# Kernel tuning notes

Measured on AMD Instinct MI355X. Metric: run time of the kernel, lower is better.

The kernel has to match this reference:

```python
import jax, jax.numpy as jnp
import numpy as np

N_EMBD = 1024
N_HEAD = 16
HEAD_DIM = N_EMBD // N_HEAD


def setup_inputs() -> dict:
    key = jax.random.key(0)
    ks = jax.random.split(key, 5)
    B, S = 2, 2048
    scale = 0.02
    return {
        "hidden_states": jax.random.normal(ks[0], (B, S, N_EMBD), dtype=jnp.float32),
        "w_attn": jax.random.normal(ks[1], (N_EMBD, 3 * N_EMBD), dtype=jnp.float32) * scale,
        "b_attn": jnp.zeros((3 * N_EMBD,), dtype=jnp.float32),
        "w_proj": jax.random.normal(ks[2], (N_EMBD, N_EMBD), dtype=jnp.float32) * scale,
        "b_proj": jnp.zeros((N_EMBD,), dtype=jnp.float32),
    }


def reference(hidden_states, w_attn, b_attn, w_proj, b_proj):
    B, S, _ = hidden_states.shape
    qkv = hidden_states @ w_attn + b_attn                     # [B,S,3E]
    q, k, v = jnp.split(qkv, 3, axis=-1)                      # each [B,S,E]

    def split_heads(t):  # [B,S,E] -> [B,H,S,D]
        return t.reshape(B, S, N_HEAD, HEAD_DIM).transpose(0, 2, 1, 3)

    q, k, v = split_heads(q), split_heads(k), split_heads(v)

    scores = jnp.einsum("bhqd,bhkd->bhqk", q, k) / np.sqrt(HEAD_DIM).astype(np.float32)
    causal = jnp.tril(jnp.ones((S, S), dtype=bool))
    scores = jnp.where(causal[None, None], scores, jnp.float32(-jnp.inf))
    attn = jax.nn.softmax(scores, axis=-1)                    # [B,H,S,S]
    out = jnp.einsum("bhqk,bhkd->bhqd", attn, v)              # [B,H,S,D]
    out = out.transpose(0, 2, 1, 3).reshape(B, S, N_EMBD)     # merge heads
    out = out @ w_proj + b_proj
    return out
```

## Files before the change

kernel.cpp:

```cpp
#include <hip/hip_runtime.h>
#include <hip/hip_bf16.h>


typedef __attribute__((ext_vector_type(4))) float  float4v;
typedef __attribute__((ext_vector_type(8))) short  short8v;
typedef __attribute__((ext_vector_type(4))) short  short4v;

#define ATT_SCALE 0.18033688011112042f

__device__ __forceinline__ short f2bf(float f) {
  union { float f; unsigned u; } v; v.f = f;
  unsigned r = v.u + 0x7fffu + ((v.u >> 16) & 1u);
  return (short)(r >> 16);
}
__device__ __forceinline__ float bf2f(short s) {
  union { unsigned u; float f; } v; v.u = ((unsigned)(unsigned short)s) << 16;
  return v.f;
}

__device__ __forceinline__ short4v pack_bf16x4(float a, float b, float c, float d) {
  unsigned x0 = __builtin_bit_cast(unsigned, a) + 0x8000u;
  unsigned x1 = __builtin_bit_cast(unsigned, b) + 0x8000u;
  unsigned x2 = __builtin_bit_cast(unsigned, c) + 0x8000u;
  unsigned x3 = __builtin_bit_cast(unsigned, d) + 0x8000u;
  union { unsigned u[2]; short4v s; } r;
  r.u[0] = __builtin_amdgcn_perm(x1, x0, 0x07060302);
  r.u[1] = __builtin_amdgcn_perm(x3, x2, 0x07060302);
  return r.s;
}

__device__ __forceinline__ short4v cvt_pk_bf16x4(float a, float b, float c, float d) {
  union { unsigned u[2]; short4v s; } r;
  asm("v_cvt_pk_bf16_f32 %0, %1, %2" : "=v"(r.u[0]) : "v"(a), "v"(b));
  asm("v_cvt_pk_bf16_f32 %0, %1, %2" : "=v"(r.u[1]) : "v"(c), "v"(d));
  return r.s;
}

__device__ __forceinline__ void gl_lds16(const void* g, void* l) {
  __builtin_amdgcn_global_load_lds(
      (const __attribute__((address_space(1))) unsigned*)g,
      (__attribute__((address_space(3))) unsigned*)l, 16, 0, 0);
}

__global__ __launch_bounds__(256) void prep_kernel(
    const float* __restrict__ hidden, const float* __restrict__ w_attn,
    const float* __restrict__ w_proj, short* __restrict__ hA,
    short* __restrict__ wqkvT, short* __restrict__ wprojT) {
  __shared__ float tile[32][33];
  const int bx = blockIdx.x, t = threadIdx.x;
  if (bx < 4096) {
    const size_t i = ((size_t)bx * 256 + t) * 4;
    float4v v = *(const float4v*)(hidden + i);
    short4v o;
    #pragma unroll
    for (int k = 0; k < 4; k++) o[k] = f2bf(v[k]);
    *(short4v*)(hA + i) = o;
    return;
  }
  const float* in; short* out; int R, C, cx, cy;
  if (bx < 4096 + 3072) {
    in = w_attn; out = wqkvT; R = 1024; C = 3072;
    cx = (bx - 4096) % 96; cy = (bx - 4096) / 96;
  } else {
    in = w_proj; out = wprojT; R = 1024; C = 1024;
    cx = (bx - 7168) % 32; cy = (bx - 7168) / 32;
  }
  const int tx = t & 31, ty = t >> 5;
  const int c0 = cx * 32, r0 = cy * 32;
  #pragma unroll
  for (int i = 0; i < 4; i++)
    tile[ty + i * 8][tx] = in[(size_t)(r0 + ty + i * 8) * C + c0 + tx];
  __syncthreads();
  #pragma unroll
  for (int i = 0; i < 4; i++) {
    const int cc = ty + i * 8;
    out[(size_t)(c0 + cc) * R + r0 + tx] = f2bf(tile[tx][cc]);
  }
}

template<int RB, int MODE>
__global__ __launch_bounds__(256) void gemm_bt(
    const short* __restrict__ A, const short* __restrict__ Bt,
    const float* __restrict__ bias, void* __restrict__ Cout,
    short* __restrict__ vA, int M, int N, int K)
{
  __shared__ short As[3][RB][32];
  __shared__ short Bs[3][128][32];
  const int MI = RB / 32;
  const int t    = threadIdx.x;
  const int lane = t & 63;
  const int wave = t >> 6;
  const int wm   = (wave >> 1) * (RB / 2);
  const int wn   = (wave & 1) * 64;
  const int l16  = lane & 15;
  const int quad = lane >> 4;
  const int row0 = blockIdx.y * RB;
  const int col0 = blockIdx.x * 128;

  float4v acc[MI][4] = {};

  const int srow = lane >> 2;
  const int scol = (lane & 3) * 8;
  const int gcol = ((lane & 3) ^ ((srow >> 1) & 3)) * 8;
  const int rquad = (quad ^ ((l16 >> 1) & 3)) * 8;

  const short* gA0 = A + (size_t)(row0 + wave * ((RB == 128) ? 32 : 16) + srow) * K + gcol;
  const short* gA1 = gA0 + (size_t)16 * K;
  const short* gB0 = Bt + (size_t)(col0 + wave * 32 + srow) * K + gcol;
  const short* gB1 = gB0 + (size_t)16 * K;

  const int NI = K / 32;

  auto stage = [&](int kt, int b) {
    const int k0 = kt * 32;
    if (RB == 128) {
      gl_lds16(gA0 + k0, &As[b][wave * 32 + srow][scol]);
      gl_lds16(gA1 + k0, &As[b][wave * 32 + 16 + srow][scol]);
    } else {
      gl_lds16(gA0 + k0, &As[b][(wave * 16 + srow) & (RB - 1)][scol]);
    }
    gl_lds16(gB0 + k0, &Bs[b][wave * 32 + srow][scol]);
    gl_lds16(gB1 + k0, &Bs[b][wave * 32 + 16 + srow][scol]);
  };

  stage(0, 0);
  stage(1, 1);
  if (RB == 128) asm volatile("s_waitcnt vmcnt(4)" ::: "memory");
  else           asm volatile("s_waitcnt vmcnt(3)" ::: "memory");
  __builtin_amdgcn_s_barrier();
  __builtin_amdgcn_sched_barrier(0);

  int buf = 0;
  for (int i = 0; i < NI; i++) {
    if (i + 2 < NI) stage(i + 2, (buf + 2 >= 3) ? buf - 1 : buf + 2);

    short8v af[MI], bf[4];
    #pragma unroll
    for (int ii = 0; ii < MI; ii++)
      af[ii] = *(const short8v*)&As[buf][wm + ii * 16 + l16][rquad];
    #pragma unroll
    for (int j = 0; j < 4; j++)
      bf[j] = *(const short8v*)&Bs[buf][wn + j * 16 + l16][rquad];
    #pragma unroll
    for (int ii = 0; ii < MI; ii++)
      #pragma unroll
      for (int j = 0; j < 4; j++)
        acc[ii][j] = __builtin_amdgcn_mfma_f32_16x16x32_bf16(af[ii], bf[j], acc[ii][j], 0, 0, 0);

    if (i + 1 < NI) {
      if (i + 2 < NI) {
        if (RB == 128) asm volatile("s_waitcnt vmcnt(4)" ::: "memory");
        else           asm volatile("s_waitcnt vmcnt(3)" ::: "memory");
      } else {
        asm volatile("s_waitcnt vmcnt(0)" ::: "memory");
      }
      __builtin_amdgcn_s_barrier();
      __builtin_amdgcn_sched_barrier(0);
    }
    buf = (buf >= 2) ? 0 : buf + 1;
  }

  if (MODE == 2 && col0 >= 2048) {
    const int b  = row0 >> 11;
    const int hh = ((col0 - 2048) >> 6) + (wn >> 6);
    const int kt = ((row0 & 2047) >> 6) + (wm >> 6);
    short* vbase = vA + ((size_t)((b * 16 + hh) * 32 + kt) * 8) * 512;
    #pragma unroll
    for (int j = 0; j < 4; j++) {
      const float bv = bias[col0 + wn + j * 16 + l16];
      #pragma unroll
      for (int kwp = 0; kwp < 2; kwp++) {
        short8v s8;
        #pragma unroll
        for (int kw = 0; kw < 2; kw++) {
          short4v q4 = pack_bf16x4(acc[kwp * 2 + kw][j][0] + bv,
                                   acc[kwp * 2 + kw][j][1] + bv,
                                   acc[kwp * 2 + kw][j][2] + bv,
                                   acc[kwp * 2 + kw][j][3] + bv);
          #pragma unroll
          for (int r = 0; r < 4; r++) s8[kw * 4 + r] = q4[r];
        }
        *(short8v*)(vbase + ((size_t)(kwp * 4 + j) * 64 + lane) * 8) = s8;
      }
    }
    return;
  }

  #pragma unroll
  for (int j = 0; j < 4; j++) {
    const int col = col0 + wn + j * 16 + l16;
    const float sc = (MODE == 2 && col < 1024) ? ATT_SCALE : 1.0f;
    const float bv = bias[col];
    #pragma unroll
    for (int i = 0; i < MI; i++) {
      #pragma unroll
      for (int r = 0; r < 4; r++) {
        const int row = row0 + wm + i * 16 + quad * 4 + r;
        const float v = (acc[i][j][r] + bv) * sc;
        if (MODE == 2) ((short*)Cout)[(size_t)row * N + col] = f2bf(v);
        else           ((float*)Cout)[(size_t)row * N + col] = v;
      }
    }
  }
}

__global__ __launch_bounds__(256, 2) void attn_mfma(
    const short* __restrict__ qkv, const short* __restrict__ vA,
    short* __restrict__ P0, short* __restrict__ P1, float* __restrict__ lp)
{
  __shared__ short KA[2][8 * 512];

  const int bh = blockIdx.y;
  const int b = bh >> 4, h = bh & 15;
  const int s = 79 - blockIdx.x;
  int qt = 0, sbase = 0;
  for (;;) { const int nc = (qt >> 3) + 1; if (s < sbase + nc) break; sbase += nc; qt++; }
  const int c = s - sbase;
  const int kt0  = c * 8;
  const int kend = min(qt + 1, kt0 + 8);

  const int t = threadIdx.x;
  const int lane = t & 63, w = t >> 6;
  const int l16 = lane & 15, quad = lane >> 4;

  const size_t base = (size_t)b * 2048 * 3072;
  const int qoff = h * 64, koff = 1024 + h * 64;
  const int qg = qt * 64 + w * 16 + l16;

  short8v qf[2];
  #pragma unroll
  for (int ks = 0; ks < 2; ks++)
    qf[ks] = *(const short8v*)(qkv + base + (size_t)qg * 3072 + qoff + ks * 32 + quad * 8);

  float4v O[4] = {};
  float l = 0.0f;

  const int id0 = w * 2, id1 = id0 + 1;
  const int jm0 = id0 & 3, ks0 = id0 >> 2;
  const int jm1 = id1 & 3, ks1 = id1 >> 2;
  const short* kg0 = qkv + base + (size_t)(jm0 * 16 + l16) * 3072 + koff + ks0 * 32 + quad * 8;
  const short* kg1 = qkv + base + (size_t)(jm1 * 16 + l16) * 3072 + koff + ks1 * 32 + quad * 8;
  const short* vg  = vA + (size_t)(bh * 32) * 4096 + lane * 8;

  gl_lds16(kg0 + (size_t)kt0 * 64 * 3072, &KA[0][id0 * 512 + lane * 8]);
  gl_lds16(kg1 + (size_t)kt0 * 64 * 3072, &KA[0][id1 * 512 + lane * 8]);

  for (int kt = kt0; kt < kend; kt++) {
    const int buf = (kt - kt0) & 1;
    __syncthreads();

    short8v vv[8];
    #pragma unroll
    for (int id = 0; id < 8; id++)
      vv[id] = *(const short8v*)(vg + (size_t)kt * 4096 + id * 512);

    if (kt + 1 < kend) {
      gl_lds16(kg0 + (size_t)(kt + 1) * 64 * 3072, &KA[buf ^ 1][id0 * 512 + lane * 8]);
      gl_lds16(kg1 + (size_t)(kt + 1) * 64 * 3072, &KA[buf ^ 1][id1 * 512 + lane * 8]);
    }

    float4v sv[4] = {};
    __builtin_amdgcn_s_setprio(1);
    #pragma unroll
    for (int ks = 0; ks < 2; ks++)
      #pragma unroll
      for (int jm = 0; jm < 4; jm++) {
        const short8v kf = *(const short8v*)&KA[buf][(ks * 4 + jm) * 512 + lane * 8];
        sv[jm] = __builtin_amdgcn_mfma_f32_16x16x32_bf16(kf, qf[ks], sv[jm], 0, 0, 0);
      }
    __builtin_amdgcn_s_setprio(0);

    if (kt == qt) {
      #pragma unroll
      for (int jm = 0; jm < 4; jm++) {
        const int kv = kt * 64 + jm * 16 + quad * 4;
        #pragma unroll
        for (int r = 0; r < 4; r++)
          if (kv + r > qg) sv[jm][r] = -INFINITY;
      }
    }

    short4v pk[4];
    #pragma unroll
    for (int jm = 0; jm < 4; jm++) {
      float p0 = __builtin_amdgcn_exp2f(sv[jm][0]);
      float p1 = __builtin_amdgcn_exp2f(sv[jm][1]);
      float p2 = __builtin_amdgcn_exp2f(sv[jm][2]);
      float p3 = __builtin_amdgcn_exp2f(sv[jm][3]);
      l += (p0 + p1) + (p2 + p3);
      pk[jm] = cvt_pk_bf16x4(p0, p1, p2, p3);
    }

    __builtin_amdgcn_s_setprio(1);
    #pragma unroll
    for (int id = 0; id < 8; id++) {
      const int kwp = id >> 2, dm = id & 3;
      const short8v v8 = vv[id];
      const short4v v0 = {v8[0], v8[1], v8[2], v8[3]};
      const short4v v1 = {v8[4], v8[5], v8[6], v8[7]};
      O[dm] = __builtin_amdgcn_mfma_f32_16x16x16bf16_1k(v0, pk[kwp * 2],     O[dm], 0, 0, 0);
      O[dm] = __builtin_amdgcn_mfma_f32_16x16x16bf16_1k(v1, pk[kwp * 2 + 1], O[dm], 0, 0, 0);
    }
    __builtin_amdgcn_s_setprio(0);
  }

  l += __shfl_xor(l, 16);
  l += __shfl_xor(l, 32);
  const int i = bh * 80 + s;
  short* pp = (i < 2048) ? (P0 + (size_t)i * 4096) : (P1 + (size_t)(i - 2048) * 4096);
  const int row = w * 16 + l16;
  if (quad == 0) lp[(size_t)i * 64 + row] = l;
  short* pr = pp + row * 64;
  #pragma unroll
  for (int dm = 0; dm < 4; dm++)
    *(short4v*)(pr + dm * 16 + quad * 4) =
        pack_bf16x4(O[dm][0], O[dm][1], O[dm][2], O[dm][3]);
}

__global__ __launch_bounds__(256) void merge_attn(
    const short* __restrict__ P0, const short* __restrict__ P1,
    const float* __restrict__ lp, short* __restrict__ aout)
{
  const int idx = blockIdx.x * 256 + threadIdx.x;
  const int q = idx >> 7;
  const int rest = idx & 127;
  const int h  = rest >> 3;
  const int dg = (rest & 7) * 8;
  const int b  = q >> 11;
  const int qr = q & 2047;
  const int qt = qr >> 6;
  const int row = qr & 63;
  const int a = qt >> 3, bq = qt & 7;
  const int off = qt + 4 * a * (a - 1) + a * bq;
  const int nc  = a + 1;
  const int bh  = b * 16 + h;

  float acc[8] = {};
  float suml = 0.0f;
  for (int c = 0; c < nc; c++) {
    const int i = bh * 80 + off + c;
    const short* pp = (i < 2048) ? (P0 + (size_t)i * 4096) : (P1 + (size_t)(i - 2048) * 4096);
    const short8v o = *(const short8v*)(pp + row * 64 + dg);
    #pragma unroll
    for (int k = 0; k < 8; k++) acc[k] += bf2f(o[k]);
    suml += lp[(size_t)i * 64 + row];
  }
  const float inv = 1.0f / suml;
  short8v ov;
  #pragma unroll
  for (int k = 0; k < 8; k++) ov[k] = f2bf(acc[k] * inv);
  *(short8v*)(aout + (size_t)q * 1024 + h * 64 + dg) = ov;
}

extern "C" void kernel_launch(void* const* d_in, const int* in_sizes, int n_in,
                              void* d_out, int out_size, void* d_ws, size_t ws_size,
                              hipStream_t stream) {
  const float* hidden = (const float*)d_in[0];
  const float* w_attn = (const float*)d_in[1];
  const float* b_attn = (const float*)d_in[2];
  const float* w_proj = (const float*)d_in[3];
  const float* b_proj = (const float*)d_in[4];
  float* outp = (float*)d_out;

  char* ws = (char*)d_ws;
  short* hA     = (short*)(ws);
  float* lp     = (float*)(ws + 8ull  * 1024 * 1024);
  short* wqkvT  = (short*)(ws + 8ull  * 1024 * 1024);
  short* wprojT = (short*)(ws + 14ull * 1024 * 1024);
  short* qkvb   = (short*)(ws + 16ull * 1024 * 1024);
  short* vAbuf  = (short*)(ws + 40ull * 1024 * 1024);
  short* aout   = (short*)(ws + 40ull * 1024 * 1024);
  short* P0     = (short*)d_out;

  prep_kernel<<<8192, 256, 0, stream>>>(hidden, w_attn, w_proj, hA, wqkvT, wprojT);
  gemm_bt<128, 2><<<dim3(24, 32), 256, 0, stream>>>(hA, wqkvT, b_attn, qkvb, vAbuf, 4096, 3072, 1024);
  attn_mfma<<<dim3(80, 32), 256, 0, stream>>>(qkvb, vAbuf, P0, hA, lp);
  merge_attn<<<2048, 256, 0, stream>>>(P0, hA, lp, aout);
  gemm_bt<64, 0><<<dim3(8, 64), 256, 0, stream>>>(aout, wprojT, b_proj, outp, nullptr, 4096, 1024, 1024);
}
```

Baseline: 206.1 us.

## Add 256x256-tile 8-wave QKV GEMM with swizzled LDS and ping-pong pipeline

Replaces the 128x128 QKV projection GEMM with a dedicated 512-thread kernel that computes 256x256 output tiles using 64-wide K slices. Tiles are staged through XOR-swizzled, double-buffered LDS and interleaved with MFMA phases under s_setprio and fine-grained barriers. The aim is more reuse per loaded byte, fewer global loads and better overlap of loads with MFMA. The trade-off is only 192 blocks on the device and high register and LDS pressure. The generic GEMM is reduced to the fp32 output path.

```diff
diff --git a/kernel.cpp b/kernel.cpp
--- a/kernel.cpp
+++ b/kernel.cpp
@@ -75,6 +75,165 @@
   for (int i = 0; i < 4; i++) {
     const int cc = ty + i * 8;
     out[(size_t)(c0 + cc) * R + r0 + tx] = f2bf(tile[tx][cc]);
+  }
+}
+
+__global__ __launch_bounds__(512, 2) void gemm_qkv256(
+    const short* __restrict__ A, const short* __restrict__ Bt,
+    const float* __restrict__ bias, short* __restrict__ qkv,
+    short* __restrict__ vA)
+{
+  __shared__ short As[2][256][64];
+  __shared__ short Bs[2][256][64];
+  const int K = 1024;
+  const int t = threadIdx.x;
+  const int lane = t & 63, w = t >> 6;
+  const int wm2 = w >> 2, wn4 = w & 3;
+  const int l16 = lane & 15, quad = lane >> 4;
+  const int e7 = l16 & 7;
+  const int row0 = blockIdx.y * 256;
+  const int col0 = blockIdx.x * 256;
+
+  float4v acc[8][4] = {};
+
+  const int srow = w * 8 + (lane >> 3);
+  const int slog = (lane & 7) ^ (lane >> 3);
+  const short* gA = A + (size_t)(row0 + srow) * K + slog * 8;
+  const short* gB = Bt + (size_t)(col0 + srow) * K + slog * 8;
+  const int sdst = (lane & 7) * 8;
+
+  auto stageA = [&](int b, int qd, int kt) {
+    gl_lds16(gA + (size_t)qd * 64 * K + kt * 64,
+             &As[b][qd * 64 + w * 8 + (lane >> 3)][sdst]);
+  };
+  auto stageB = [&](int b, int qd, int kt) {
+    gl_lds16(gB + (size_t)qd * 64 * K + kt * 64,
+             &Bs[b][qd * 64 + w * 8 + (lane >> 3)][sdst]);
+  };
+
+  short8v af[4], bf0[4], bf1[4];
+  auto ldA = [&](int b, int mh, int ks) {
+    #pragma unroll
+    for (int m = 0; m < 4; m++) {
+      const int row = wm2 * 128 + mh * 64 + m * 16 + l16;
+      af[m] = *(const short8v*)&As[b][row][((ks * 4 + quad) ^ e7) * 8];
+    }
+  };
+  auto ldB = [&](short8v* bf, int b, int ks) {
+    #pragma unroll
+    for (int n = 0; n < 4; n++) {
+      const int row = wn4 * 64 + n * 16 + l16;
+      bf[n] = *(const short8v*)&Bs[b][row][((ks * 4 + quad) ^ e7) * 8];
+    }
+  };
+  auto mm = [&](int mb, short8v* bf) {
+    __builtin_amdgcn_s_setprio(1);
+    #pragma unroll
+    for (int m = 0; m < 4; m++)
+      #pragma unroll
+      for (int n = 0; n < 4; n++)
+        acc[mb + m][n] =
+            __builtin_amdgcn_mfma_f32_16x16x32_bf16(af[m], bf[n], acc[mb + m][n], 0, 0, 0);
+    __builtin_amdgcn_s_setprio(0);
+  };
+  auto sync_mfma = [&]() {
+    __builtin_amdgcn_sched_barrier(0);
+    __builtin_amdgcn_s_barrier();
+    asm volatile("s_waitcnt lgkmcnt(0)" ::: "memory");
+    __builtin_amdgcn_sched_barrier(0);
+  };
+  auto endp = [&]() {
+    __builtin_amdgcn_sched_barrier(0);
+    __builtin_amdgcn_s_barrier();
+    __builtin_amdgcn_sched_barrier(0);
+  };
+
+  #pragma unroll
+  for (int qd = 0; qd < 4; qd++) stageA(0, qd, 0);
+  #pragma unroll
+  for (int qd = 0; qd < 4; qd++) stageB(0, qd, 0);
+  #pragma unroll
+  for (int qd = 0; qd < 4; qd++) stageB(1, qd, 1);
+  asm volatile("s_waitcnt vmcnt(4)" ::: "memory");
+  __builtin_amdgcn_s_barrier();
+  __builtin_amdgcn_sched_barrier(0);
+
+  const int NIT = K / 128;
+  #pragma unroll 1
+  for (int it = 0; it < NIT; it++) {
+    const bool st = (it < NIT - 1);
+    const int t1 = 2 * it + 1, t2 = 2 * it + 2, t3 = 2 * it + 3;
+
+    ldA(0, 0, 0); ldB(bf0, 0, 0);
+    stageA(1, 0, t1); stageA(1, 1, t1);
+    sync_mfma(); mm(0, bf0); endp();
+    ldA(0, 0, 1); ldB(bf1, 0, 1);
+    stageA(1, 2, t1); stageA(1, 3, t1);
+    sync_mfma(); mm(0, bf1); endp();
+    ldA(0, 1, 0);
+    if (st) { stageB(0, 0, t2); stageB(0, 1, t2); }
+    sync_mfma(); mm(4, bf0); endp();
+    ldA(0, 1, 1);
+    if (st) { stageB(0, 2, t2); stageB(0, 3, t2); }
+    if (st) asm volatile("s_waitcnt vmcnt(4)" ::: "memory");
+    else    asm volatile("s_waitcnt vmcnt(0)" ::: "memory");
+    sync_mfma(); mm(4, bf1); endp();
+
+    ldA(1, 0, 0); ldB(bf0, 1, 0);
+    if (st) { stageA(0, 0, t2); stageA(0, 1, t2); }
+    sync_mfma(); mm(0, bf0); endp();
+    ldA(1, 0, 1); ldB(bf1, 1, 1);
+    if (st) { stageA(0, 2, t2); stageA(0, 3, t2); }
+    sync_mfma(); mm(0, bf1); endp();
+    ldA(1, 1, 0);
+    if (st) { stageB(1, 0, t3); stageB(1, 1, t3); }
+    sync_mfma(); mm(4, bf0); endp();
+    ldA(1, 1, 1);
+    if (st) { stageB(1, 2, t3); stageB(1, 3, t3); }
+    if (st) asm volatile("s_waitcnt vmcnt(4)" ::: "memory");
+    sync_mfma(); mm(4, bf1); endp();
+  }
+
+  if (col0 >= 2048) {
+    const int b  = row0 >> 11;
+    const int hh = ((col0 - 2048) >> 6) + wn4;
+    #pragma unroll
+    for (int ktl = 0; ktl < 2; ktl++) {
+      const int kt = ((row0 & 2047) >> 6) + wm2 * 2 + ktl;
+      short* vbase = vA + ((size_t)((b * 16 + hh) * 32 + kt) * 8) * 512;
+      #pragma unroll
+      for (int j = 0; j < 4; j++) {
+        const float bv = bias[col0 + wn4 * 64 + j * 16 + l16];
+        #pragma unroll
+        for (int kwp = 0; kwp < 2; kwp++) {
+          short8v s8;
+          #pragma unroll
+          for (int kw = 0; kw < 2; kw++) {
+            const int mi = ktl * 4 + kwp * 2 + kw;
+            short4v q4 = pack_bf16x4(acc[mi][j][0] + bv, acc[mi][j][1] + bv,
+                                     acc[mi][j][2] + bv, acc[mi][j][3] + bv);
+            #pragma unroll
+            for (int r = 0; r < 4; r++) s8[kw * 4 + r] = q4[r];
+          }
+          *(short8v*)(vbase + ((size_t)(kwp * 4 + j) * 64 + lane) * 8) = s8;
+        }
+      }
+    }
+    return;
+  }
+  #pragma unroll
+  for (int j = 0; j < 4; j++) {
+    const int col = col0 + wn4 * 64 + j * 16 + l16;
+    const float sc = (col < 1024) ? ATT_SCALE : 1.0f;
+    const float bv = bias[col];
+    #pragma unroll
+    for (int mi = 0; mi < 8; mi++) {
+      #pragma unroll
+      for (int r = 0; r < 4; r++) {
+        const int row = row0 + wm2 * 128 + mi * 16 + quad * 4 + r;
+        qkv[(size_t)row * 3072 + col] = f2bf((acc[mi][j][r] + bv) * sc);
+      }
+    }
   }
 }
 
@@ -160,45 +319,16 @@
     buf = (buf >= 2) ? 0 : buf + 1;
   }
 
-  if (MODE == 2 && col0 >= 2048) {
-    const int b  = row0 >> 11;
-    const int hh = ((col0 - 2048) >> 6) + (wn >> 6);
-    const int kt = ((row0 & 2047) >> 6) + (wm >> 6);
-    short* vbase = vA + ((size_t)((b * 16 + hh) * 32 + kt) * 8) * 512;
-    #pragma unroll
-    for (int j = 0; j < 4; j++) {
-      const float bv = bias[col0 + wn + j * 16 + l16];
-      #pragma unroll
-      for (int kwp = 0; kwp < 2; kwp++) {
-        short8v s8;
-        #pragma unroll
-        for (int kw = 0; kw < 2; kw++) {
-          short4v q4 = pack_bf16x4(acc[kwp * 2 + kw][j][0] + bv,
-                                   acc[kwp * 2 + kw][j][1] + bv,
-                                   acc[kwp * 2 + kw][j][2] + bv,
-                                   acc[kwp * 2 + kw][j][3] + bv);
-          #pragma unroll
-          for (int r = 0; r < 4; r++) s8[kw * 4 + r] = q4[r];
-        }
-        *(short8v*)(vbase + ((size_t)(kwp * 4 + j) * 64 + lane) * 8) = s8;
-      }
-    }
-    return;
-  }
-
   #pragma unroll
   for (int j = 0; j < 4; j++) {
     const int col = col0 + wn + j * 16 + l16;
-    const float sc = (MODE == 2 && col < 1024) ? ATT_SCALE : 1.0f;
     const float bv = bias[col];
     #pragma unroll
     for (int i = 0; i < MI; i++) {
       #pragma unroll
       for (int r = 0; r < 4; r++) {
         const int row = row0 + wm + i * 16 + quad * 4 + r;
-        const float v = (acc[i][j][r] + bv) * sc;
-        if (MODE == 2) ((short*)Cout)[(size_t)row * N + col] = f2bf(v);
-        else           ((float*)Cout)[(size_t)row * N + col] = v;
+        ((float*)Cout)[(size_t)row * N + col] = acc[i][j][r] + bv;
       }
     }
   }
@@ -373,7 +503,7 @@
   short* P0     = (short*)d_out;
 
   prep_kernel<<<8192, 256, 0, stream>>>(hidden, w_attn, w_proj, hA, wqkvT, wprojT);
-  gemm_bt<128, 2><<<dim3(24, 32), 256, 0, stream>>>(hA, wqkvT, b_attn, qkvb, vAbuf, 4096, 3072, 1024);
+  gemm_qkv256<<<dim3(12, 16), 512, 0, stream>>>(hA, wqkvT, b_attn, qkvb, vAbuf);
   attn_mfma<<<dim3(80, 32), 256, 0, stream>>>(qkvb, vAbuf, P0, hA, lp);
   merge_attn<<<2048, 256, 0, stream>>>(P0, hA, lp, aout);
   gemm_bt<64, 0><<<dim3(8, 64), 256, 0, stream>>>(aout, wprojT, b_proj, outp, nullptr, 4096, 1024, 1024);
```

Measured after the change: 193.6 us. -6.1%, faster.
